# Optimization experiments

Hardware: AMD Instinct MI355X
Metric: run time of the kernel (lower is better)

The kernel has to match this reference:

```python
import jax, jax.numpy as jnp
import numpy as np

N = 50000      # nodes
E = 800000     # edges (before self-loops)
F_IN = 64      # num_features
HID = 32       # hidden_channels
HEADS = 4
CLS = 3
NEG_SLOPE = 0.2  # PyG GATConv default


def setup_inputs() -> dict:
    key = jax.random.key(0)
    ks = jax.random.split(key, 12)
    s = 0.1
    return {
        "x": jax.random.normal(ks[0], (N, F_IN), jnp.float32),
        "W1": jax.random.normal(ks[1], (F_IN, HEADS * HID), jnp.float32) * s,
        "att_src1": jax.random.normal(ks[2], (HEADS, HID), jnp.float32) * s,
        "att_dst1": jax.random.normal(ks[3], (HEADS, HID), jnp.float32) * s,
        "b1": jnp.zeros((HEADS * HID,), jnp.float32),
        "W2": jax.random.normal(ks[4], (HEADS * HID, HID), jnp.float32) * s,
        "att_src2": jax.random.normal(ks[5], (1, HID), jnp.float32) * s,
        "att_dst2": jax.random.normal(ks[6], (1, HID), jnp.float32) * s,
        "b2": jnp.zeros((HID,), jnp.float32),
        "linW": jax.random.normal(ks[7], (HID, CLS), jnp.float32) * s,
        "linb": jnp.zeros((CLS,), jnp.float32),
        "edge_index": jax.random.randint(ks[8], (2, E), 0, N, dtype=jnp.int64),
    }


def _gat_conv(x, W, att_src, att_dst, bias, src, dst, heads):
    """PyG GATConv (eval mode, self-loops pre-added in src/dst)."""
    n = x.shape[0]
    h = (x @ W).reshape(n, heads, -1)                      # [N,H,C]
    a_src = jnp.sum(h * att_src, axis=-1)                  # [N,H]
    a_dst = jnp.sum(h * att_dst, axis=-1)                  # [N,H]
    e = jax.nn.leaky_relu(a_src[src] + a_dst[dst], NEG_SLOPE)  # [E,H]
    # segment softmax over destination node
    m = jax.ops.segment_max(e, dst, num_segments=n)
    p = jnp.exp(e - m[dst])
    denom = jax.ops.segment_sum(p, dst, num_segments=n)
    alpha = p / denom[dst]                                 # [E,H]
    msg = h[src] * alpha[:, :, None]                       # [E,H,C]
    out = jax.ops.segment_sum(msg, dst, num_segments=n)    # [N,H,C]
    return out.reshape(n, -1) + bias                       # concat heads


def reference(x, W1, att_src1, att_dst1, b1, W2, att_src2, att_dst2, b2, linW, linb, edge_index):
    n = x.shape[0]
    loop = jnp.arange(n, dtype=edge_index.dtype)
    src = jnp.concatenate([edge_index[0], loop])  # add self-loops (PyG default)
    dst = jnp.concatenate([edge_index[1], loop])
    h = _gat_conv(x, W1, att_src1, att_dst1, b1, src, dst, HEADS)
    h = jax.nn.elu(h)
    h = _gat_conv(h, W2, att_src2, att_dst2, b2, src, dst, 1)
    g = jnp.mean(h, axis=0, keepdims=True)        # batch is None path
    logits = g @ linW + linb                      # [1, CLS]
    return jax.nn.softmax(logits, axis=1)
```

## Files before the change

kernel.cpp:

```cpp
#include <hip/hip_runtime.h>
#include <hip/hip_fp16.h>
#include <math.h>

#define NEG_SLOPE 0.2f
#define CAP 64
#define SCB 2048

static __device__ __forceinline__ void atomAdd(float* a, float v) {
    unsafeAtomicAdd(a, v);
}

static __device__ __forceinline__ bool edges_are_i64(const int* __restrict__ ei) {
    return (ei[1] | ei[3] | ei[5] | ei[7]) == 0;
}
static __device__ __forceinline__ int ldsrc(const int* __restrict__ ei, int e, int E, bool i64) {
    return i64 ? ei[2 * e] : ei[e];
}
static __device__ __forceinline__ int lddst(const int* __restrict__ ei, int e, int E, bool i64) {
    return i64 ? ei[2 * (E + e)] : ei[E + e];
}

__global__ __launch_bounds__(256) void scatter_k(const int* __restrict__ ei,
                                                 int* __restrict__ deg,
                                                 unsigned short* __restrict__ col,
                                                 int E, int N) {
    const int tid = threadIdx.x;
    const int grp = blockIdx.x & 7;
    const int bin = blockIdx.x >> 3;
    const int nb  = gridDim.x >> 3;
    const bool i64 = edges_are_i64(ei);
    const int ET = E + N;
    const int d0 = (int)((long long)grp * N / 8);
    const int d1 = (int)((long long)(grp + 1) * N / 8);
    for (int e = bin * 256 + tid; e < ET; e += nb * 256) {
        int s, d;
        if (e < E) { s = ldsrc(ei, e, E, i64); d = lddst(ei, e, E, i64); }
        else       { s = d = e - E; }
        if (d >= d0 && d < d1) {
            int pos = atomicAdd(&deg[d], 1);
            if (pos < CAP) col[d * CAP + pos] = (unsigned short)s;
        }
    }
}

__global__ __launch_bounds__(256, 4) void gemm1_k(const float* __restrict__ x,
                                                  const float* __restrict__ W,
                                                  const float* __restrict__ aws,
                                                  const float* __restrict__ awd,
                                                  __half* __restrict__ h,
                                                  float* __restrict__ as_,
                                                  float* __restrict__ ad_, int N) {
    __shared__ float Ws[64 * 128];
    __shared__ float xs[32 * 64];
    const int tid = threadIdx.x;
    const int cg = tid & 31, rg = tid >> 5;
    const int r0 = blockIdx.x * 32;
#pragma unroll 1
    for (int i = tid; i < 8192; i += 256) Ws[i] = W[i];
    {
        const float* src = x + (size_t)r0 * 64;
        const int limit = (N - r0) * 64;
#pragma unroll 1
        for (int i = tid * 4; i < 2048; i += 1024) {
            float4 v = (i < limit) ? *(const float4*)(src + i) : make_float4(0, 0, 0, 0);
            *(float4*)(xs + i) = v;
        }
    }
    __syncthreads();

    float acc[4][4] = {};
#pragma unroll 2
    for (int k = 0; k < 64; k += 4) {
        float4 w0 = *(const float4*)(Ws + (k + 0) * 128 + cg * 4);
        float4 w1 = *(const float4*)(Ws + (k + 1) * 128 + cg * 4);
        float4 w2 = *(const float4*)(Ws + (k + 2) * 128 + cg * 4);
        float4 w3 = *(const float4*)(Ws + (k + 3) * 128 + cg * 4);
        float4 xv[4];
#pragma unroll
        for (int q = 0; q < 4; ++q) xv[q] = *(const float4*)(xs + (rg * 4 + q) * 64 + k);
#pragma unroll
        for (int q = 0; q < 4; ++q) {
            float4 xq = xv[q];
            acc[q][0] += xq.x * w0.x + xq.y * w1.x + xq.z * w2.x + xq.w * w3.x;
            acc[q][1] += xq.x * w0.y + xq.y * w1.y + xq.z * w2.y + xq.w * w3.y;
            acc[q][2] += xq.x * w0.z + xq.y * w1.z + xq.z * w2.z + xq.w * w3.z;
            acc[q][3] += xq.x * w0.w + xq.y * w1.w + xq.z * w2.w + xq.w * w3.w;
        }
    }

    const int jbase = cg * 4;
    const int head = cg >> 3;
    const float a0 = aws[jbase], a1 = aws[jbase + 1], a2 = aws[jbase + 2], a3 = aws[jbase + 3];
    const float d0 = awd[jbase], d1 = awd[jbase + 1], d2 = awd[jbase + 2], d3 = awd[jbase + 3];
    float ps[4], pd[4];
#pragma unroll
    for (int q = 0; q < 4; ++q) {
        ps[q] = acc[q][0] * a0 + acc[q][1] * a1 + acc[q][2] * a2 + acc[q][3] * a3;
        pd[q] = acc[q][0] * d0 + acc[q][1] * d1 + acc[q][2] * d2 + acc[q][3] * d3;
        int row = r0 + rg * 4 + q;
        if (row < N) {
            __half hv[4];
            hv[0] = __float2half(acc[q][0]); hv[1] = __float2half(acc[q][1]);
            hv[2] = __float2half(acc[q][2]); hv[3] = __float2half(acc[q][3]);
            *(uint2*)(h + (size_t)row * 128 + jbase) = *(uint2*)hv;
        }
    }
#pragma unroll
    for (int off = 4; off; off >>= 1) {
#pragma unroll
        for (int q = 0; q < 4; ++q) {
            ps[q] += __shfl_down(ps[q], off, 8);
            pd[q] += __shfl_down(pd[q], off, 8);
        }
    }
    if ((cg & 7) == 0) {
#pragma unroll
        for (int q = 0; q < 4; ++q) {
            int row = r0 + rg * 4 + q;
            if (row < N) { as_[row * 4 + head] = ps[q]; ad_[row * 4 + head] = pd[q]; }
        }
    }
}

__global__ __launch_bounds__(256, 4) void gemm2_k(const __half* __restrict__ hact,
                                                  const float* __restrict__ W,
                                                  const float* __restrict__ aws,
                                                  const float* __restrict__ awd,
                                                  __half* __restrict__ h2,
                                                  float* __restrict__ as_,
                                                  float* __restrict__ ad_, int N) {
    __shared__ float Ws[128 * 32];
    __shared__ float xs[128 * 68];
    const int tid = threadIdx.x;
    const int cg = tid & 7, rg = tid >> 3;
    const int r0 = blockIdx.x * 128;
    for (int i = tid; i < 4096; i += 256) Ws[i] = W[i];

    float acc[4][4] = {};
#pragma unroll 1
    for (int p = 0; p < 2; ++p) {
        __syncthreads();
#pragma unroll 2
        for (int i = tid * 4; i < 8192; i += 1024) {
            int row = i >> 6, kk = i & 63;
            float4 v = make_float4(0, 0, 0, 0);
            if (r0 + row < N) {
                uint2 hv = *(const uint2*)(hact + (size_t)(r0 + row) * 128 + p * 64 + kk);
                const __half2* ph = (const __half2*)&hv;
                float2 f0 = __half22float2(ph[0]);
                float2 f1 = __half22float2(ph[1]);
                v = make_float4(f0.x, f0.y, f1.x, f1.y);
            }
            *(float4*)(xs + row * 68 + kk) = v;
        }
        __syncthreads();
#pragma unroll 2
        for (int k = 0; k < 64; k += 4) {
            float4 w0 = *(const float4*)(Ws + (p * 64 + k + 0) * 32 + cg * 4);
            float4 w1 = *(const float4*)(Ws + (p * 64 + k + 1) * 32 + cg * 4);
            float4 w2 = *(const float4*)(Ws + (p * 64 + k + 2) * 32 + cg * 4);
            float4 w3 = *(const float4*)(Ws + (p * 64 + k + 3) * 32 + cg * 4);
            float4 xv[4];
#pragma unroll
            for (int q = 0; q < 4; ++q) xv[q] = *(const float4*)(xs + (rg * 4 + q) * 68 + k);
#pragma unroll
            for (int q = 0; q < 4; ++q) {
                float4 xq = xv[q];
                acc[q][0] += xq.x * w0.x + xq.y * w1.x + xq.z * w2.x + xq.w * w3.x;
                acc[q][1] += xq.x * w0.y + xq.y * w1.y + xq.z * w2.y + xq.w * w3.y;
                acc[q][2] += xq.x * w0.z + xq.y * w1.z + xq.z * w2.z + xq.w * w3.z;
                acc[q][3] += xq.x * w0.w + xq.y * w1.w + xq.z * w2.w + xq.w * w3.w;
            }
        }
    }

    const int jbase = cg * 4;
    const float a0 = aws[jbase], a1 = aws[jbase + 1], a2 = aws[jbase + 2], a3 = aws[jbase + 3];
    const float d0 = awd[jbase], d1 = awd[jbase + 1], d2 = awd[jbase + 2], d3 = awd[jbase + 3];
    float ps[4], pd[4];
#pragma unroll
    for (int q = 0; q < 4; ++q) {
        ps[q] = acc[q][0] * a0 + acc[q][1] * a1 + acc[q][2] * a2 + acc[q][3] * a3;
        pd[q] = acc[q][0] * d0 + acc[q][1] * d1 + acc[q][2] * d2 + acc[q][3] * d3;
        int row = r0 + rg * 4 + q;
        if (row < N) {
            __half hv[4];
            hv[0] = __float2half(acc[q][0]); hv[1] = __float2half(acc[q][1]);
            hv[2] = __float2half(acc[q][2]); hv[3] = __float2half(acc[q][3]);
            *(uint2*)(h2 + (size_t)row * 32 + jbase) = *(uint2*)hv;
        }
    }
#pragma unroll
    for (int off = 4; off; off >>= 1) {
#pragma unroll
        for (int q = 0; q < 4; ++q) {
            ps[q] += __shfl_down(ps[q], off, 8);
            pd[q] += __shfl_down(pd[q], off, 8);
        }
    }
    if (cg == 0) {
#pragma unroll
        for (int q = 0; q < 4; ++q) {
            int row = r0 + rg * 4 + q;
            if (row < N) { as_[row] = ps[q]; ad_[row] = pd[q]; }
        }
    }
}

template <int NB>
static __device__ __forceinline__ void p1_batch(int s, float p, const __half* __restrict__ h,
                                                int lane, float& acc0, float& acc1) {
    int su[NB];
#pragma unroll
    for (int u = 0; u < NB; ++u) su[u] = __shfl(s, u, 16);
    __half2 g[NB];
#pragma unroll
    for (int u = 0; u < NB; ++u) g[u] = *(const __half2*)(h + (size_t)su[u] * 128 + lane * 2);
    float pu[NB];
#pragma unroll
    for (int u = 0; u < NB; ++u) pu[u] = __shfl(p, u, 16);
#pragma unroll
    for (int u = 0; u < NB; ++u) {
        float2 gf = __half22float2(g[u]);
        acc0 += pu[u] * gf.x; acc1 += pu[u] * gf.y;
    }
}

__global__ __launch_bounds__(256) void pull_agg1_k(const int* __restrict__ deg,
                                                   const unsigned short* __restrict__ col,
                                                   const float* __restrict__ asrc,
                                                   const float* __restrict__ adst,
                                                   const __half* __restrict__ h,
                                                   const float* __restrict__ b1,
                                                   __half* __restrict__ hact, int N) {
    int wave = (blockIdx.x * 256 + threadIdx.x) >> 6;
    int lane = threadIdx.x & 63;
    if (wave >= N) return;
    const int d = wave;
    const int hd = lane >> 4;
    const int el = lane & 15;
    const float ad = adst[d * 4 + hd];
    const unsigned short* cl = col + d * CAP;
    int cnt = deg[d]; if (cnt > CAP) cnt = CAP;
    float acc0 = 0.0f, acc1 = 0.0f, den = 0.0f;

    for (int i = 0; i < cnt; i += 16) {
        const int r = cnt - i;
        int s = 0; float p = 0.0f;
        if (el < r) {
            s = cl[i + el];
            float v = asrc[s * 4 + hd] + ad;
            v = v > 0.0f ? v : NEG_SLOPE * v;
            p = __expf(v);
        }
        den += p;
        if (r >= 9)      p1_batch<16>(s, p, h, lane, acc0, acc1);
        else if (r >= 5) p1_batch<8>(s, p, h, lane, acc0, acc1);
        else             p1_batch<4>(s, p, h, lane, acc0, acc1);
    }
    den += __shfl_xor(den, 1, 16);
    den += __shfl_xor(den, 2, 16);
    den += __shfl_xor(den, 4, 16);
    den += __shfl_xor(den, 8, 16);

    float inv = 1.0f / den;
    float o0 = acc0 * inv + b1[lane * 2];
    float o1 = acc1 * inv + b1[lane * 2 + 1];
    o0 = o0 > 0.0f ? o0 : expm1f(o0);
    o1 = o1 > 0.0f ? o1 : expm1f(o1);
    *(__half2*)(hact + (size_t)d * 128 + lane * 2) = __floats2half2_rn(o0, o1);
}

template <int NB>
static __device__ __forceinline__ void p2_batch(int s, float p, const __half* __restrict__ h,
                                                int lane, float& acc) {
    int su[NB];
#pragma unroll
    for (int u = 0; u < NB; ++u) su[u] = __shfl(s, u, 16);
    __half g[NB];
#pragma unroll
    for (int u = 0; u < NB; ++u) g[u] = h[(size_t)su[u] * 32 + lane];
    float pu[NB];
#pragma unroll
    for (int u = 0; u < NB; ++u) pu[u] = __shfl(p, u, 16);
#pragma unroll
    for (int u = 0; u < NB; ++u) acc += pu[u] * __half2float(g[u]);
}

__global__ __launch_bounds__(256) void pull_agg2_k(const int* __restrict__ deg,
                                                   const unsigned short* __restrict__ col,
                                                   const float* __restrict__ asrc,
                                                   const float* __restrict__ adst,
                                                   const __half* __restrict__ h,
                                                   float* __restrict__ gsum, int N) {
    const int lane = threadIdx.x & 31;
    const int el = lane & 15;
    const int gloc = threadIdx.x >> 5;
    float csum = 0.0f;
    for (int d = blockIdx.x * 8 + gloc; d < N; d += gridDim.x * 8) {
        const float ad = adst[d];
        const unsigned short* cl = col + d * CAP;
        int cnt = deg[d]; if (cnt > CAP) cnt = CAP;
        float acc = 0.0f, den = 0.0f;
        for (int i = 0; i < cnt; i += 16) {
            const int r = cnt - i;
            int s = 0; float p = 0.0f;
            if (el < r) {
                s = cl[i + el];
                float v = asrc[s] + ad;
                v = v > 0.0f ? v : NEG_SLOPE * v;
                p = __expf(v);
            }
            den += p;
            if (r >= 9)      p2_batch<16>(s, p, h, lane, acc);
            else if (r >= 5) p2_batch<8>(s, p, h, lane, acc);
            else             p2_batch<4>(s, p, h, lane, acc);
        }
        den += __shfl_xor(den, 1, 16);
        den += __shfl_xor(den, 2, 16);
        den += __shfl_xor(den, 4, 16);
        den += __shfl_xor(den, 8, 16);
        csum += acc / den;
    }
    __shared__ float lds[256];
    lds[threadIdx.x] = csum;
    __syncthreads();
    if (threadIdx.x < 32) {
        float s2 = 0.0f;
#pragma unroll
        for (int g = 0; g < 8; ++g) s2 += lds[g * 32 + threadIdx.x];
        atomAdd(&gsum[threadIdx.x], s2);
    }
}

__global__ void final_k(const float* __restrict__ gsum, const float* __restrict__ b2w,
                        const float* __restrict__ linW, const float* __restrict__ linb,
                        float* __restrict__ out, int N) {
    if (threadIdx.x != 0 || blockIdx.x != 0) return;
    float g[32];
#pragma unroll
    for (int c = 0; c < 32; ++c) g[c] = gsum[c] / (float)N + b2w[c];
    float lo[3];
#pragma unroll
    for (int j = 0; j < 3; ++j) {
        float acc = linb[j];
#pragma unroll
        for (int c = 0; c < 32; ++c) acc += g[c] * linW[c * 3 + j];
        lo[j] = acc;
    }
    float mx = fmaxf(lo[0], fmaxf(lo[1], lo[2]));
    float ex[3], se = 0.0f;
#pragma unroll
    for (int j = 0; j < 3; ++j) { ex[j] = __expf(lo[j] - mx); se += ex[j]; }
#pragma unroll
    for (int j = 0; j < 3; ++j) out[j] = ex[j] / se;
}

extern "C" void kernel_launch(void* const* d_in, const int* in_sizes, int n_in,
                              void* d_out, int out_size, void* d_ws, size_t ws_size,
                              hipStream_t stream) {
    const float* x    = (const float*)d_in[0];
    const float* W1   = (const float*)d_in[1];
    const float* as1w = (const float*)d_in[2];
    const float* ad1w = (const float*)d_in[3];
    const float* b1   = (const float*)d_in[4];
    const float* W2   = (const float*)d_in[5];
    const float* as2w = (const float*)d_in[6];
    const float* ad2w = (const float*)d_in[7];
    const float* b2w  = (const float*)d_in[8];
    const float* linW = (const float*)d_in[9];
    const float* linb = (const float*)d_in[10];
    const int*   ei   = (const int*)d_in[11];

    const int N = in_sizes[0] / 64;
    const int E = in_sizes[11] / 2;

    float* ws = (float*)d_ws;
    __half* h1h  = (__half*)ws;
    __half* hacth = (__half*)(ws + (size_t)N * 64);
    float* asrc1 = ws + (size_t)N * 128;
    float* adst1 = asrc1 + (size_t)N * 4;
    float* asrc2 = adst1 + (size_t)N * 4;
    float* adst2 = asrc2 + (size_t)N;
    float* gsum  = adst2 + (size_t)N;
    __half* h2h  = (__half*)ws;
    int* deg     = (int*)(gsum + 32);
    unsigned short* col = (unsigned short*)(deg + N);

    auto cdiv = [](int a, int b) { return (a + b - 1) / b; };

    hipMemsetAsync(deg, 0, (size_t)N * sizeof(int), stream);
    hipMemsetAsync(gsum, 0, 32 * sizeof(float), stream);

    scatter_k<<<SCB, 256, 0, stream>>>(ei, deg, col, E, N);

    gemm1_k<<<cdiv(N, 32), 256, 0, stream>>>(x, W1, as1w, ad1w, h1h, asrc1, adst1, N);
    pull_agg1_k<<<cdiv(N, 4), 256, 0, stream>>>(deg, col, asrc1, adst1, h1h, b1, hacth, N);

    gemm2_k<<<cdiv(N, 128), 256, 0, stream>>>(hacth, W2, as2w, ad2w, h2h, asrc2, adst2, N);
    pull_agg2_k<<<2048, 256, 0, stream>>>(deg, col, asrc2, adst2, h2h, gsum, N);

    final_k<<<1, 64, 0, stream>>>(gsum, b2w, linW, linb, (float*)d_out, N);
}
```

Before: 245.3 us.

## Pre-partition edges by dest slice, fuse scatter into GEMM1, fold final into agg2

Adds a partition pass that sorts edges into 8 destination-slice buckets through LDS staging. The adjacency scatter then runs as extra blocks inside the first GEMM kernel, so the CSR build overlaps the GEMM. This replaces the old scatter, where each of 8 block groups read every edge and kept only its slice. The final softmax kernel is folded into pull_agg2 using a last-block counter. The cost is an extra pass that writes a bucket buffer, plus more workspace and atomics.

```diff
diff --git a/kernel.cpp b/kernel.cpp
--- a/kernel.cpp
+++ b/kernel.cpp
@@ -4,7 +4,7 @@
 
 #define NEG_SLOPE 0.2f
 #define CAP 64
-#define SCB 2048
+#define SCATB 2048
 
 static __device__ __forceinline__ void atomAdd(float* a, float v) {
     unsafeAtomicAdd(a, v);
@@ -20,39 +20,72 @@
     return i64 ? ei[2 * (E + e)] : ei[E + e];
 }
 
-__global__ __launch_bounds__(256) void scatter_k(const int* __restrict__ ei,
-                                                 int* __restrict__ deg,
-                                                 unsigned short* __restrict__ col,
-                                                 int E, int N) {
+__global__ __launch_bounds__(256) void partition_k(const int* __restrict__ ei,
+                                                   unsigned int* __restrict__ bkt,
+                                                   int* __restrict__ cur,
+                                                   int E, int N, int CAPB) {
+    __shared__ int lcnt[8], lbase[8];
+    __shared__ unsigned int lbuf[8][256];
     const int tid = threadIdx.x;
-    const int grp = blockIdx.x & 7;
-    const int bin = blockIdx.x >> 3;
-    const int nb  = gridDim.x >> 3;
     const bool i64 = edges_are_i64(ei);
     const int ET = E + N;
-    const int d0 = (int)((long long)grp * N / 8);
-    const int d1 = (int)((long long)(grp + 1) * N / 8);
-    for (int e = bin * 256 + tid; e < ET; e += nb * 256) {
-        int s, d;
-        if (e < E) { s = ldsrc(ei, e, E, i64); d = lddst(ei, e, E, i64); }
-        else       { s = d = e - E; }
-        if (d >= d0 && d < d1) {
-            int pos = atomicAdd(&deg[d], 1);
-            if (pos < CAP) col[d * CAP + pos] = (unsigned short)s;
-        }
-    }
-}
-
-__global__ __launch_bounds__(256, 4) void gemm1_k(const float* __restrict__ x,
-                                                  const float* __restrict__ W,
-                                                  const float* __restrict__ aws,
-                                                  const float* __restrict__ awd,
-                                                  __half* __restrict__ h,
-                                                  float* __restrict__ as_,
-                                                  float* __restrict__ ad_, int N) {
+    const float sliceScale = 8.0f / (float)N;
+    for (int base = blockIdx.x * 256; base < ET; base += gridDim.x * 256) {
+        if (tid < 8) lcnt[tid] = 0;
+        __syncthreads();
+        const int e = base + tid;
+        if (e < ET) {
+            int s, d;
+            if (e < E) { s = ldsrc(ei, e, E, i64); d = lddst(ei, e, E, i64); }
+            else       { s = d = e - E; }
+            int g = (int)((float)d * sliceScale);
+            g = g < 0 ? 0 : (g > 7 ? 7 : g);
+            int pos = atomicAdd(&lcnt[g], 1);
+            lbuf[g][pos] = (unsigned int)s | ((unsigned int)d << 16);
+        }
+        __syncthreads();
+        if (tid < 8) lbase[tid] = atomicAdd(&cur[tid], lcnt[tid]);
+        __syncthreads();
+        for (int g = 0; g < 8; ++g) {
+            const int n = lcnt[g], b = lbase[g];
+            for (int i = tid; i < n; i += 256) {
+                const int idx = b + i;
+                if (idx < CAPB) bkt[(size_t)g * CAPB + idx] = lbuf[g][i];
+            }
+        }
+        __syncthreads();
+    }
+}
+
+__global__ __launch_bounds__(256, 4) void ka_k(const float* __restrict__ x,
+                                               const float* __restrict__ W,
+                                               const float* __restrict__ aws,
+                                               const float* __restrict__ awd,
+                                               __half* __restrict__ h,
+                                               float* __restrict__ as_,
+                                               float* __restrict__ ad_,
+                                               const unsigned int* __restrict__ bkt,
+                                               const int* __restrict__ cur,
+                                               int* __restrict__ deg,
+                                               unsigned short* __restrict__ col,
+                                               int N, int G1, int CAPB) {
     __shared__ float Ws[64 * 128];
     __shared__ float xs[32 * 64];
     const int tid = threadIdx.x;
+    if ((int)blockIdx.x >= G1) {
+        const int grp = blockIdx.x & 7;
+        const int bin = (blockIdx.x - G1) >> 3;
+        const int nb  = (gridDim.x - G1) >> 3;
+        int cnt = cur[grp]; if (cnt > CAPB) cnt = CAPB;
+        const unsigned int* bk = bkt + (size_t)grp * CAPB;
+        for (int i = bin * 256 + tid; i < cnt; i += nb * 256) {
+            const unsigned int u = bk[i];
+            const int d = (int)(u >> 16), s = (int)(u & 0xFFFFu);
+            int pos = atomicAdd(&deg[d], 1);
+            if (pos < CAP) col[d * CAP + pos] = (unsigned short)s;
+        }
+        return;
+    }
     const int cg = tid & 31, rg = tid >> 5;
     const int r0 = blockIdx.x * 32;
 #pragma unroll 1
@@ -292,10 +325,16 @@
                                                    const float* __restrict__ asrc,
                                                    const float* __restrict__ adst,
                                                    const __half* __restrict__ h,
-                                                   float* __restrict__ gsum, int N) {
-    const int lane = threadIdx.x & 31;
+                                                   float* __restrict__ gsum,
+                                                   int* __restrict__ counter,
+                                                   const float* __restrict__ b2w,
+                                                   const float* __restrict__ linW,
+                                                   const float* __restrict__ linb,
+                                                   float* __restrict__ out, int N) {
+    const int tid = threadIdx.x;
+    const int lane = tid & 31;
     const int el = lane & 15;
-    const int gloc = threadIdx.x >> 5;
+    const int gloc = tid >> 5;
     float csum = 0.0f;
     for (int d = blockIdx.x * 8 + gloc; d < N; d += gridDim.x * 8) {
         const float ad = adst[d];
@@ -323,37 +362,43 @@
         csum += acc / den;
     }
     __shared__ float lds[256];
-    lds[threadIdx.x] = csum;
+    lds[tid] = csum;
     __syncthreads();
-    if (threadIdx.x < 32) {
+    if (tid < 32) {
         float s2 = 0.0f;
 #pragma unroll
-        for (int g = 0; g < 8; ++g) s2 += lds[g * 32 + threadIdx.x];
-        atomAdd(&gsum[threadIdx.x], s2);
-    }
-}
-
-__global__ void final_k(const float* __restrict__ gsum, const float* __restrict__ b2w,
-                        const float* __restrict__ linW, const float* __restrict__ linb,
-                        float* __restrict__ out, int N) {
-    if (threadIdx.x != 0 || blockIdx.x != 0) return;
-    float g[32];
-#pragma unroll
-    for (int c = 0; c < 32; ++c) g[c] = gsum[c] / (float)N + b2w[c];
-    float lo[3];
-#pragma unroll
-    for (int j = 0; j < 3; ++j) {
-        float acc = linb[j];
-#pragma unroll
-        for (int c = 0; c < 32; ++c) acc += g[c] * linW[c * 3 + j];
-        lo[j] = acc;
-    }
-    float mx = fmaxf(lo[0], fmaxf(lo[1], lo[2]));
-    float ex[3], se = 0.0f;
-#pragma unroll
-    for (int j = 0; j < 3; ++j) { ex[j] = __expf(lo[j] - mx); se += ex[j]; }
-#pragma unroll
-    for (int j = 0; j < 3; ++j) out[j] = ex[j] / se;
+        for (int g = 0; g < 8; ++g) s2 += lds[g * 32 + tid];
+        atomAdd(&gsum[tid], s2);
+    }
+    __threadfence();
+    __syncthreads();
+    __shared__ int isLast;
+    if (tid == 0) isLast = (atomicAdd(counter, 1) == (int)gridDim.x - 1);
+    __syncthreads();
+    if (isLast) {
+        __shared__ float gv[32];
+        if (tid < 32) gv[tid] = unsafeAtomicAdd(&gsum[tid], 0.0f);
+        __syncthreads();
+        if (tid == 0) {
+            float g[32];
+#pragma unroll
+            for (int c = 0; c < 32; ++c) g[c] = gv[c] / (float)N + b2w[c];
+            float lo[3];
+#pragma unroll
+            for (int j = 0; j < 3; ++j) {
+                float acc = linb[j];
+#pragma unroll
+                for (int c = 0; c < 32; ++c) acc += g[c] * linW[c * 3 + j];
+                lo[j] = acc;
+            }
+            float mx = fmaxf(lo[0], fmaxf(lo[1], lo[2]));
+            float ex[3], se = 0.0f;
+#pragma unroll
+            for (int j = 0; j < 3; ++j) { ex[j] = __expf(lo[j] - mx); se += ex[j]; }
+#pragma unroll
+            for (int j = 0; j < 3; ++j) out[j] = ex[j] / se;
+        }
+    }
 }
 
 extern "C" void kernel_launch(void* const* d_in, const int* in_sizes, int n_in,
@@ -374,31 +419,37 @@
 
     const int N = in_sizes[0] / 64;
     const int E = in_sizes[11] / 2;
+    const int CAPB = (E + N) / 8 + 8192;
 
     float* ws = (float*)d_ws;
-    __half* h1h  = (__half*)ws;
+    __half* h1h   = (__half*)ws;
     __half* hacth = (__half*)(ws + (size_t)N * 64);
     float* asrc1 = ws + (size_t)N * 128;
     float* adst1 = asrc1 + (size_t)N * 4;
     float* asrc2 = adst1 + (size_t)N * 4;
     float* adst2 = asrc2 + (size_t)N;
     float* gsum  = adst2 + (size_t)N;
+    int* counter = (int*)(gsum + 32);
+    int* cur     = (int*)(gsum + 33);
+    int* deg     = cur + 8;
+    unsigned short* col = (unsigned short*)(deg + N);
+    unsigned int* bkt = (unsigned int*)(col + (size_t)N * CAP);
     __half* h2h  = (__half*)ws;
-    int* deg     = (int*)(gsum + 32);
-    unsigned short* col = (unsigned short*)(deg + N);
 
     auto cdiv = [](int a, int b) { return (a + b - 1) / b; };
+    const int G1 = cdiv(N, 32);
 
     hipMemsetAsync(deg, 0, (size_t)N * sizeof(int), stream);
-    hipMemsetAsync(gsum, 0, 32 * sizeof(float), stream);
-
-    scatter_k<<<SCB, 256, 0, stream>>>(ei, deg, col, E, N);
-
-    gemm1_k<<<cdiv(N, 32), 256, 0, stream>>>(x, W1, as1w, ad1w, h1h, asrc1, adst1, N);
+    hipMemsetAsync(gsum, 0, 41 * sizeof(float), stream);
+
+    partition_k<<<1024, 256, 0, stream>>>(ei, bkt, cur, E, N, CAPB);
+
+    ka_k<<<G1 + SCATB, 256, 0, stream>>>(x, W1, as1w, ad1w, h1h, asrc1, adst1,
+                                         bkt, cur, deg, col, N, G1, CAPB);
+
     pull_agg1_k<<<cdiv(N, 4), 256, 0, stream>>>(deg, col, asrc1, adst1, h1h, b1, hacth, N);
 
     gemm2_k<<<cdiv(N, 128), 256, 0, stream>>>(hacth, W2, as2w, ad2w, h2h, asrc2, adst2, N);
-    pull_agg2_k<<<2048, 256, 0, stream>>>(deg, col, asrc2, adst2, h2h, gsum, N);
-
-    final_k<<<1, 64, 0, stream>>>(gsum, b2w, linW, linb, (float*)d_out, N);
-}
+    pull_agg2_k<<<2048, 256, 0, stream>>>(deg, col, asrc2, adst2, h2h, gsum, counter,
+                                          b2w, linW, linb, (float*)d_out, N);
+}
```

New measurement: 391.1 us. 1.59x slower.
